# Optimization experiments

Hardware: AMD Instinct MI355X
Metric: run time of the kernel (lower is better)

## Reference

```python
import jax, jax.numpy as jnp
import numpy as np

H = 8          # num_heads
SPARSITY = 0.1


def setup_inputs() -> dict:
    key = jax.random.key(0)
    ks = jax.random.split(key, 16)
    B, S, D = 2, 2048, 1024
    g2 = H * H  # 64, distill width
    std = 0.02
    inp = {
        "x":   jax.random.normal(ks[0], (B, S, D), dtype=jnp.float32),
        "Wq":  jax.random.normal(ks[1], (D, D)) * std, "bq": jnp.zeros((D,)),
        "Wk":  jax.random.normal(ks[2], (D, D)) * std, "bk": jnp.zeros((D,)),
        "Wv":  jax.random.normal(ks[3], (D, D)) * std, "bv": jnp.zeros((D,)),
        "Wo":  jax.random.normal(ks[4], (D, D)) * std, "bo": jnp.zeros((D,)),
        "Wd":  jax.random.normal(ks[5], (g2, g2)) * std, "bd": jnp.zeros((g2,)),
        "Wg":  jax.random.normal(ks[6], (g2, D)) * std,  "bg": jnp.zeros((g2,)),
        "Wgp": jax.random.normal(ks[7], (D, g2)) * std,  "bgp": jnp.zeros((D,)),
    }
    return inp


def reference(x, Wq, bq, Wk, bk, Wv, bv, Wo, bo, Wd, bd, Wg, bg, Wgp, bgp):
    B, S, D = x.shape
    Dh = D // H
    scale = Dh ** -0.5
    k = max(int(S * SPARSITY), 1)

    def heads(W, b):  # [B,S,D] -> [B,H,S,Dh]
        return (x @ W.T + b).reshape(B, S, H, Dh).transpose(0, 2, 1, 3)

    Q, K, V = heads(Wq, bq), heads(Wk, bk), heads(Wv, bv)

    scores = jnp.einsum("bhqd,bhkd->bhqk", Q, K) * scale       # [B,H,S,S]
    # per-row top-k threshold (k-th largest value of each query row)
    thr = jax.lax.top_k(scores, k)[0][..., k - 1:k]              # [B,H,S,1]
    masked = jnp.where(scores >= thr, scores, -jnp.inf)
    probs = jax.nn.softmax(masked, axis=-1)
    attn = jnp.einsum("bhqk,bhkd->bhqd", probs, V)               # [B,H,S,Dh]
    attn = attn.transpose(0, 2, 1, 3).reshape(B, S, D)           # [B,S,D]

    g2 = H * H
    distilled = (attn.reshape(-1, g2) @ Wd.T + bd).reshape(B, S, D)

    gate = jax.nn.sigmoid(x.mean(axis=1) @ Wg.T + bg)            # [B,g2]
    gate = (gate @ Wgp.T + bgp)[:, None, :]                      # [B,1,D]

    mixed = gate * distilled + (1.0 - gate) * attn
    return mixed @ Wo.T + bo
```

## Files before the change

kernel.cpp:

```cpp
#include <hip/hip_runtime.h>

typedef __attribute__((ext_vector_type(8))) short bf16x8;
typedef __attribute__((ext_vector_type(4))) float f32x4;
typedef __attribute__((ext_vector_type(4))) unsigned int u32x4;

#define DEVINL __device__ __forceinline__

DEVINL unsigned short f2bf(float f){
  unsigned int u = __float_as_uint(f);
  unsigned int r = (u + 0x7FFFu + ((u >> 16) & 1u)) >> 16;
  return (unsigned short)r;
}
DEVINL float bf2f(unsigned short h){ return __uint_as_float(((unsigned int)h) << 16); }
DEVINL unsigned int fkey(float f){
  unsigned int u = __float_as_uint(f);
  return (u & 0x80000000u) ? ~u : (u | 0x80000000u);
}
DEVINL float fkeyinv(unsigned int k){
  unsigned int u = (k & 0x80000000u) ? (k & 0x7FFFFFFFu) : ~k;
  return __uint_as_float(u);
}
DEVINL unsigned int cvtpk(float lo, float hi){
  unsigned int r;
  asm("v_cvt_pk_bf16_f32 %0, %1, %2" : "=v"(r) : "v"(lo), "v"(hi));
  return r;
}

__global__ void prep_split_kernel(const float* __restrict__ src,
                                  unsigned short* __restrict__ hi,
                                  unsigned short* __restrict__ lo, int n){
  int i = blockIdx.x * 256 + threadIdx.x;
  if (i >= n) return;
  float f = src[i];
  unsigned short h = f2bf(f);
  hi[i] = h;
  if (lo) lo[i] = f2bf(f - bf2f(h));
}

template<bool SPLIT, int EPI>
__global__ __launch_bounds__(256) void gemm_kernel(
    const unsigned short* __restrict__ Ah, const unsigned short* __restrict__ Al,
    const unsigned short* __restrict__ Bh, const unsigned short* __restrict__ Bl,
    const float* __restrict__ bias0, const float* __restrict__ bias1, const float* __restrict__ bias2,
    unsigned short* __restrict__ qh, unsigned short* __restrict__ ql,
    unsigned short* __restrict__ kh, unsigned short* __restrict__ kl,
    unsigned short* __restrict__ vT, float* __restrict__ outf)
{
  const int K = 1024;
  __shared__ __align__(16) unsigned short sAh[128*40];
  __shared__ __align__(16) unsigned short sBh[128*40];
  __shared__ __align__(16) unsigned short sAl[SPLIT ? 128*40 : 8];
  __shared__ __align__(16) unsigned short sBl[SPLIT ? 128*40 : 8];

  const int tid = threadIdx.x;
  const int lane = tid & 63;
  const int w = tid >> 6;
  const int wr = w >> 1, wc = w & 1;
  const int l16 = lane & 15, lg = lane >> 4;
  const int bm = blockIdx.x, bn = blockIdx.y;

  f32x4 acc[4][4];
  #pragma unroll
  for (int i = 0; i < 4; i++)
    #pragma unroll
    for (int j = 0; j < 4; j++)
      acc[i][j] = (f32x4){0.f,0.f,0.f,0.f};

  for (int kt = 0; kt < K/32; ++kt){
    __syncthreads();
    #pragma unroll
    for (int c = 0; c < 2; c++){
      int lin = tid*16 + c*8;
      int row = lin >> 5, col = lin & 31;
      *(bf16x8*)&sAh[row*40+col] = *(const bf16x8*)&Ah[(size_t)(bm*128+row)*K + kt*32 + col];
      *(bf16x8*)&sBh[row*40+col] = *(const bf16x8*)&Bh[(size_t)(bn*128+row)*K + kt*32 + col];
      if constexpr (SPLIT){
        *(bf16x8*)&sAl[row*40+col] = *(const bf16x8*)&Al[(size_t)(bm*128+row)*K + kt*32 + col];
        *(bf16x8*)&sBl[row*40+col] = *(const bf16x8*)&Bl[(size_t)(bn*128+row)*K + kt*32 + col];
      }
    }
    __syncthreads();

    bf16x8 afh[4], afl[4], bfh[4], bfl[4];
    #pragma unroll
    for (int mi = 0; mi < 4; mi++){
      int off = (wr*64 + mi*16 + l16)*40 + lg*8;
      afh[mi] = *(const bf16x8*)&sAh[off];
      if constexpr (SPLIT) afl[mi] = *(const bf16x8*)&sAl[off];
    }
    #pragma unroll
    for (int ni = 0; ni < 4; ni++){
      int off = (wc*64 + ni*16 + l16)*40 + lg*8;
      bfh[ni] = *(const bf16x8*)&sBh[off];
      if constexpr (SPLIT) bfl[ni] = *(const bf16x8*)&sBl[off];
    }
    #pragma unroll
    for (int mi = 0; mi < 4; mi++)
      #pragma unroll
      for (int ni = 0; ni < 4; ni++){
        acc[mi][ni] = __builtin_amdgcn_mfma_f32_16x16x32_bf16(afh[mi], bfh[ni], acc[mi][ni], 0, 0, 0);
        if constexpr (SPLIT){
          acc[mi][ni] = __builtin_amdgcn_mfma_f32_16x16x32_bf16(afh[mi], bfl[ni], acc[mi][ni], 0, 0, 0);
          acc[mi][ni] = __builtin_amdgcn_mfma_f32_16x16x32_bf16(afl[mi], bfh[ni], acc[mi][ni], 0, 0, 0);
        }
      }
  }

  if constexpr (EPI == 0){
    const int wsel = (bn * 128) >> 10;
    const float* bias = (wsel == 0) ? bias0 : (wsel == 1) ? bias1 : bias2;
    #pragma unroll
    for (int mi = 0; mi < 4; mi++)
      #pragma unroll
      for (int ni = 0; ni < 4; ni++)
        #pragma unroll
        for (int i = 0; i < 4; i++){
          int m = bm*128 + wr*64 + mi*16 + lg*4 + i;
          int ng = bn*128 + wc*64 + ni*16 + l16;
          int n = ng & 1023;
          float v = acc[mi][ni][i] + bias[n];
          int b = m >> 11, s = m & 2047;
          int h = n >> 7, dh = n & 127;
          size_t base = (size_t)(b*8 + h)*262144;
          if (wsel == 2){
            size_t off = base + (size_t)(s>>5)*4096 + (dh>>4)*512
                       + (size_t)((((s>>3)&3)*16 + (dh&15))*8 + (s&7));
            vT[off] = f2bf(v);
          } else {
            size_t off = base + (size_t)(s>>4)*2048 + (dh>>5)*512
                       + (size_t)((((dh>>3)&3)*16 + (s&15))*8 + (dh&7));
            unsigned short hv = f2bf(v);
            if (wsel == 0){ qh[off] = hv; ql[off] = f2bf(v - bf2f(hv)); }
            else          { kh[off] = hv; kl[off] = f2bf(v - bf2f(hv)); }
          }
        }
  } else {
    #pragma unroll
    for (int mi = 0; mi < 4; mi++)
      #pragma unroll
      for (int ni = 0; ni < 4; ni++)
        #pragma unroll
        for (int i = 0; i < 4; i++){
          int m = bm*128 + wr*64 + mi*16 + lg*4 + i;
          int n = bn*128 + wc*64 + ni*16 + l16;
          outf[(size_t)m*1024 + n] = acc[mi][ni][i] + bias0[n];
        }
  }
}

__global__ __launch_bounds__(512, 4) void attn_kernel(
    const unsigned short* __restrict__ qh, const unsigned short* __restrict__ ql,
    const unsigned short* __restrict__ kh, const unsigned short* __restrict__ kl,
    const unsigned short* __restrict__ vT, float* __restrict__ attn_out)
{
  __shared__ __align__(16) float red[8][16][132];
  __shared__ float rpartm[8][16], rpartd[8][16];
  __shared__ unsigned int prefixv[16], kremv[16];
  unsigned int* hist = (unsigned int*)red;

  const int tid = threadIdx.x;
  const int lane = tid & 63;
  const int w = tid >> 6;
  const int l16 = lane & 15, lg = lane >> 4;
  const int swz = (blockIdx.x & 7) * 256 + (blockIdx.x >> 3);
  const int bh = swz >> 7, qb = swz & 127;
  const float scale = 0.08838834764831845f;

  const size_t base = (size_t)bh*262144;

  const size_t qpb = base + (size_t)qb*2048 + lane*8;
  bf16x8 aqh[4], aql[4];
  #pragma unroll
  for (int kk = 0; kk < 4; kk++){
    aqh[kk] = *(const bf16x8*)&qh[qpb + kk*512];
    aql[kk] = *(const bf16x8*)&ql[qpb + kk*512];
  }

  f32x4 acc[16];
  #pragma unroll
  for (int nt = 0; nt < 16; nt++){
    f32x4 a0 = (f32x4){0.f,0.f,0.f,0.f};
    f32x4 a1 = (f32x4){0.f,0.f,0.f,0.f};
    const size_t kb = base + (size_t)(w*16 + nt)*2048 + lane*8;
    __builtin_amdgcn_s_setprio(1);
    #pragma unroll
    for (int kk = 0; kk < 4; kk++){
      bf16x8 kbh = *(const bf16x8*)&kh[kb + kk*512];
      bf16x8 kbl = *(const bf16x8*)&kl[kb + kk*512];
      a0 = __builtin_amdgcn_mfma_f32_16x16x32_bf16(kbh, aqh[kk], a0, 0, 0, 0);
      a1 = __builtin_amdgcn_mfma_f32_16x16x32_bf16(kbh, aql[kk], a1, 0, 0, 0);
      a1 = __builtin_amdgcn_mfma_f32_16x16x32_bf16(kbl, aqh[kk], a1, 0, 0, 0);
    }
    __builtin_amdgcn_s_setprio(0);
    #pragma unroll
    for (int i = 0; i < 4; i++) acc[nt][i] = (a0[i] + a1[i]) * scale;
  }

  {
    float rm = -3.4e38f;
    #pragma unroll
    for (int nt = 0; nt < 16; nt++)
      #pragma unroll
      for (int i = 0; i < 4; i++) rm = fmaxf(rm, acc[nt][i]);
    rm = fmaxf(rm, __shfl_xor(rm, 16, 64));
    rm = fmaxf(rm, __shfl_xor(rm, 32, 64));
    if (lane < 16) rpartm[w][lane] = rm;
  }
  if (tid < 16){ prefixv[tid] = 0u; kremv[tid] = 204u; }

  #pragma unroll
  for (int nt = 0; nt < 16; nt++)
    #pragma unroll
    for (int i = 0; i < 4; i++)
      acc[nt][i] = __uint_as_float(fkey(acc[nt][i]));

  const int hco = (w >> 1) * (16*257);
  for (int pass = 3; pass >= 0; pass--){
    const int shift = pass*8;
    __syncthreads();
    for (int j = tid; j < 4*16*257; j += 512) hist[j] = 0u;
    __syncthreads();
    const unsigned int pf = prefixv[l16];
    const unsigned int mhi = (pass == 3) ? 0u : (0xFFFFFFFFu << (shift + 8));
    #pragma unroll
    for (int nt = 0; nt < 16; nt++)
      #pragma unroll
      for (int i = 0; i < 4; i++){
        unsigned int u = __float_as_uint(acc[nt][i]);
        if ((u & mhi) == pf)
          atomicAdd(&hist[hco + l16*257 + ((u >> shift) & 255u)], 1u);
      }
    __syncthreads();
    #pragma unroll
    for (int rr = 0; rr < 2; rr++){
      int r = w*2 + rr;
      unsigned int krem = kremv[r];
      unsigned int pfx  = prefixv[r];
      unsigned int cl[4], s4 = 0;
      #pragma unroll
      for (int t = 0; t < 4; t++){
        int idx = r*257 + 255 - 4*lane - t;
        cl[t] = hist[idx] + hist[16*257 + idx] + hist[2*16*257 + idx] + hist[3*16*257 + idx];
        s4 += cl[t];
      }
      unsigned int inc = s4;
      #pragma unroll
      for (int off = 1; off < 64; off <<= 1){
        unsigned int v = __shfl_up((int)inc, off, 64);
        if (lane >= off) inc += v;
      }
      unsigned int cb = inc - s4;
      #pragma unroll
      for (int t = 0; t < 4; t++){
        if (krem > cb && krem <= cb + cl[t]){
          int d = 255 - 4*lane - t;
          prefixv[r] = pfx | ((unsigned int)d << shift);
          kremv[r]   = krem - cb;
        }
        cb += cl[t];
      }
    }
  }
  __syncthreads();

  const unsigned int th = prefixv[l16];
  float rmax = rpartm[0][l16];
  #pragma unroll
  for (int w8 = 1; w8 < 8; w8++) rmax = fmaxf(rmax, rpartm[w8][l16]);
  const int src01 = ((lg & 1) << 5) + l16;
  const int src23 = src01 + 16;
  const size_t vb0 = base + (size_t)(w*8)*4096 + lane*8;
  float dn = 0.f;
  f32x4 pacc[8];
  #pragma unroll
  for (int dt = 0; dt < 8; dt++) pacc[dt] = (f32x4){0.f,0.f,0.f,0.f};
  #pragma unroll
  for (int t = 0; t < 8; t++){
    float p[8];
    #pragma unroll
    for (int j = 0; j < 4; j++){
      unsigned int u = __float_as_uint(acc[2*t][j]);
      p[j] = (u >= th) ? __expf(fkeyinv(u) - rmax) : 0.f;
    }
    #pragma unroll
    for (int j = 0; j < 4; j++){
      unsigned int u = __float_as_uint(acc[2*t+1][j]);
      p[4+j] = (u >= th) ? __expf(fkeyinv(u) - rmax) : 0.f;
    }
    unsigned int d0 = cvtpk(p[0], p[1]), d1 = cvtpk(p[2], p[3]);
    unsigned int d2 = cvtpk(p[4], p[5]), d3 = cvtpk(p[6], p[7]);
    dn += __uint_as_float(d0 << 16) + __uint_as_float(d0 & 0xFFFF0000u)
        + __uint_as_float(d1 << 16) + __uint_as_float(d1 & 0xFFFF0000u)
        + __uint_as_float(d2 << 16) + __uint_as_float(d2 & 0xFFFF0000u)
        + __uint_as_float(d3 << 16) + __uint_as_float(d3 & 0xFFFF0000u);
    unsigned int A0 = (unsigned int)__shfl((int)d0, src01, 64);
    unsigned int A1 = (unsigned int)__shfl((int)d1, src01, 64);
    unsigned int A2 = (unsigned int)__shfl((int)d0, src23, 64);
    unsigned int A3 = (unsigned int)__shfl((int)d1, src23, 64);
    unsigned int B0 = (unsigned int)__shfl((int)d2, src01, 64);
    unsigned int B1 = (unsigned int)__shfl((int)d3, src01, 64);
    unsigned int B2 = (unsigned int)__shfl((int)d2, src23, 64);
    unsigned int B3 = (unsigned int)__shfl((int)d3, src23, 64);
    u32x4 pdv = (lg < 2) ? (u32x4){A0, A1, A2, A3} : (u32x4){B0, B1, B2, B3};
    bf16x8 pa = __builtin_bit_cast(bf16x8, pdv);
    __builtin_amdgcn_s_setprio(1);
    #pragma unroll
    for (int dt = 0; dt < 8; dt++){
      bf16x8 bv = *(const bf16x8*)&vT[vb0 + (size_t)t*4096 + dt*512];
      pacc[dt] = __builtin_amdgcn_mfma_f32_16x16x32_bf16(pa, bv, pacc[dt], 0, 0, 0);
    }
    __builtin_amdgcn_s_setprio(0);
  }
  dn += __shfl_xor(dn, 16, 64);
  dn += __shfl_xor(dn, 32, 64);
  if (lane < 16) rpartd[w][lane] = dn;

  #pragma unroll
  for (int dt = 0; dt < 8; dt++)
    #pragma unroll
    for (int i = 0; i < 4; i++)
      red[w][lg*4 + i][dt*16 + l16] = pacc[dt][i];
  __syncthreads();

  {
    const int q = tid >> 5;
    const int c0 = (tid & 31) * 4;
    f32x4 s0 = (f32x4){0.f,0.f,0.f,0.f};
    #pragma unroll
    for (int w8 = 0; w8 < 8; w8++)
      s0 += *(const f32x4*)&red[w8][q][c0];
    float dnm = 0.f;
    #pragma unroll
    for (int w8 = 0; w8 < 8; w8++) dnm += rpartd[w8][q];
    const int b = bh >> 3, h = bh & 7;
    float* op = &attn_out[((size_t)b*2048 + qb*16 + q)*1024 + h*128 + c0];
    f32x4 o0;
    #pragma unroll
    for (int i = 0; i < 4; i++) o0[i] = s0[i] / dnm;
    *(f32x4*)op = o0;
  }
}

__global__ void mean_partial_kernel(const float* __restrict__ x, float* __restrict__ partial){
  int b = blockIdx.x >> 5, scn = blockIdx.x & 31;
  int tid = threadIdx.x;
  #pragma unroll
  for (int dc = 0; dc < 4; dc++){
    int d = dc*256 + tid;
    float s = 0.f;
    for (int ss = 0; ss < 64; ss++) s += x[((size_t)b*2048 + scn*64 + ss)*1024 + d];
    partial[((size_t)b*32 + scn)*1024 + d] = s;
  }
}

__global__ __launch_bounds__(256) void gate_kernel(const float* __restrict__ partial,
    const float* __restrict__ Wg, const float* __restrict__ bg,
    const float* __restrict__ Wgp, const float* __restrict__ bgp,
    float* __restrict__ gate){
  __shared__ float xm[2][1024];
  __shared__ float gb[2][64];
  int tid = threadIdx.x;
  for (int idx = tid; idx < 2048; idx += 256){
    int b = idx >> 10, d = idx & 1023;
    float s = 0.f;
    for (int scn = 0; scn < 32; scn++) s += partial[((size_t)b*32 + scn)*1024 + d];
    xm[b][d] = s * (1.f/2048.f);
  }
  __syncthreads();
  if (tid < 128){
    int b = tid >> 6, j = tid & 63;
    float s = bg[j];
    for (int d = 0; d < 1024; d++) s += xm[b][d] * Wg[j*1024 + d];
    gb[b][j] = 1.f / (1.f + __expf(-s));
  }
  __syncthreads();
  for (int idx = tid; idx < 2048; idx += 256){
    int b = idx >> 10, d = idx & 1023;
    float s = bgp[d];
    for (int j = 0; j < 64; j++) s += gb[b][j] * Wgp[d*64 + j];
    gate[idx] = s;
  }
}

__global__ __launch_bounds__(256) void mix_kernel(const float* __restrict__ attn,
    const float* __restrict__ Wd, const float* __restrict__ bd,
    const float* __restrict__ gate,
    unsigned short* __restrict__ mixedh, unsigned short* __restrict__ mixedl){
  __shared__ float sWdT[64*64];
  __shared__ float arow[1024];
  int tid = threadIdx.x;
  for (int i = tid; i < 4096; i += 256){
    int m = i >> 6, cc = i & 63;
    sWdT[i] = Wd[cc*64 + m];
  }
  int rbase = blockIdx.x * 16;
  for (int rr = 0; rr < 16; rr++){
    int row = rbase + rr;
    __syncthreads();
    for (int i = tid; i < 1024; i += 256) arow[i] = attn[(size_t)row*1024 + i];
    __syncthreads();
    int b = row >> 11;
    #pragma unroll
    for (int c4 = 0; c4 < 4; c4++){
      int dcol = c4*256 + tid;
      int j = dcol >> 6, cc = dcol & 63;
      float y = bd[cc];
      for (int m = 0; m < 64; m++) y += arow[j*64 + m] * sWdT[m*64 + cc];
      float g = gate[b*1024 + dcol];
      float mv = g*y + (1.f - g)*arow[dcol];
      unsigned short hv = f2bf(mv);
      mixedh[(size_t)row*1024 + dcol] = hv;
      mixedl[(size_t)row*1024 + dcol] = f2bf(mv - bf2f(hv));
    }
  }
}

extern "C" void kernel_launch(void* const* d_in, const int* in_sizes, int n_in,
                              void* d_out, int out_size, void* d_ws, size_t ws_size,
                              hipStream_t stream){
  (void)in_sizes; (void)n_in; (void)out_size; (void)ws_size;
  const float* x   = (const float*)d_in[0];
  const float* Wq  = (const float*)d_in[1];
  const float* bq  = (const float*)d_in[2];
  const float* Wk  = (const float*)d_in[3];
  const float* bk  = (const float*)d_in[4];
  const float* Wv  = (const float*)d_in[5];
  const float* bv  = (const float*)d_in[6];
  const float* Wo  = (const float*)d_in[7];
  const float* bo  = (const float*)d_in[8];
  const float* Wd  = (const float*)d_in[9];
  const float* bd  = (const float*)d_in[10];
  const float* Wg  = (const float*)d_in[11];
  const float* bg  = (const float*)d_in[12];
  const float* Wgp = (const float*)d_in[13];
  const float* bgp = (const float*)d_in[14];
  float* out = (float*)d_out;

  const size_t MiB = 1048576;
  char* ws = (char*)d_ws;
  unsigned short* xh     = (unsigned short*)(ws + 0*MiB);
  unsigned short* xl     = (unsigned short*)(ws + 8*MiB);
  float*          attnws = (float*)(ws + 0*MiB);
  unsigned short* whi    = (unsigned short*)(ws + 16*MiB);
  unsigned short* wlo    = (unsigned short*)(ws + 22*MiB);
  unsigned short* wohi   = (unsigned short*)(ws + 16*MiB);
  unsigned short* wolo   = (unsigned short*)(ws + 18*MiB);
  float*          partial= (float*)(ws + 20*MiB);
  float*          gatews = (float*)(ws + 20*MiB + 262144);
  unsigned short* qh_    = (unsigned short*)(ws + 28*MiB);
  unsigned short* ql_    = (unsigned short*)(ws + 36*MiB);
  unsigned short* mixedh = (unsigned short*)(ws + 28*MiB);
  unsigned short* mixedl = (unsigned short*)(ws + 36*MiB);
  unsigned short* kh_    = (unsigned short*)(ws + 44*MiB);
  unsigned short* kl_    = (unsigned short*)(ws + 52*MiB);
  unsigned short* vT_    = (unsigned short*)(ws + 60*MiB);

  prep_split_kernel<<<16384, 256, 0, stream>>>(x,  xh, xl, 4194304);
  prep_split_kernel<<<4096,  256, 0, stream>>>(Wq, whi,           wlo,           1048576);
  prep_split_kernel<<<4096,  256, 0, stream>>>(Wk, whi + 1048576, wlo + 1048576, 1048576);
  prep_split_kernel<<<4096,  256, 0, stream>>>(Wv, whi + 2097152, wlo + 2097152, 1048576);

  gemm_kernel<true, 0><<<dim3(32, 24), 256, 0, stream>>>(
      xh, xl, whi, wlo, bq, bk, bv, qh_, ql_, kh_, kl_, vT_, nullptr);

  prep_split_kernel<<<4096,  256, 0, stream>>>(Wo, wohi, wolo, 1048576);

  attn_kernel<<<2048, 512, 0, stream>>>(qh_, ql_, kh_, kl_, vT_, attnws);

  mean_partial_kernel<<<64, 256, 0, stream>>>(x, partial);
  gate_kernel<<<1, 256, 0, stream>>>(partial, Wg, bg, Wgp, bgp, gatews);

  mix_kernel<<<256, 256, 0, stream>>>(attnws, Wd, bd, gatews, mixedh, mixedl);

  gemm_kernel<true, 1><<<dim3(32, 8), 256, 0, stream>>>(
      mixedh, mixedl, wohi, wolo, bo, nullptr, nullptr,
      nullptr, nullptr, nullptr, nullptr, nullptr, out);
}
```

Measured before the change: 494.3 us.

## Use direct global-to-LDS loads in GEMM and parallelize gate computation

The GEMM tile loads now go through global_load_lds, which writes from global memory straight into LDS without passing through registers. The padded 40-element LDS row stride becomes an unpadded 32, which may add bank conflicts on the fragment reads. The gate path is also split: the mean reduction uses 256 blocks instead of 64, and the single-block gate kernel becomes two kernels that use wave-level shuffle reductions and vectorized weight loads, removing a serial one-block bottleneck.

After: 473.8 us. 4.1% less time.

```diff
diff --git a/kernel.cpp b/kernel.cpp
--- a/kernel.cpp
+++ b/kernel.cpp
@@ -24,6 +24,10 @@
   unsigned int r;
   asm("v_cvt_pk_bf16_f32 %0, %1, %2" : "=v"(r) : "v"(lo), "v"(hi));
   return r;
+}
+DEVINL void gload16(void* lds, const void* g){
+  __builtin_amdgcn_global_load_lds((const __attribute__((address_space(1))) void*)g,
+                                   (__attribute__((address_space(3))) void*)lds, 16, 0, 0);
 }
 
 __global__ void prep_split_kernel(const float* __restrict__ src,
@@ -47,10 +51,10 @@
     unsigned short* __restrict__ vT, float* __restrict__ outf)
 {
   const int K = 1024;
-  __shared__ __align__(16) unsigned short sAh[128*40];
-  __shared__ __align__(16) unsigned short sBh[128*40];
-  __shared__ __align__(16) unsigned short sAl[SPLIT ? 128*40 : 8];
-  __shared__ __align__(16) unsigned short sBl[SPLIT ? 128*40 : 8];
+  __shared__ __align__(16) unsigned short sAh[128*32];
+  __shared__ __align__(16) unsigned short sBh[128*32];
+  __shared__ __align__(16) unsigned short sAl[SPLIT ? 128*32 : 8];
+  __shared__ __align__(16) unsigned short sBl[SPLIT ? 128*32 : 8];
 
   const int tid = threadIdx.x;
   const int lane = tid & 63;
@@ -59,6 +63,10 @@
   const int l16 = lane & 15, lg = lane >> 4;
   const int bm = blockIdx.x, bn = blockIdx.y;
 
+  const int srow = (lane >> 2);
+  const int scol = (lane & 3) * 8;
+  const int r0 = w * 32;
+
   f32x4 acc[4][4];
   #pragma unroll
   for (int i = 0; i < 4; i++)
@@ -69,14 +77,14 @@
   for (int kt = 0; kt < K/32; ++kt){
     __syncthreads();
     #pragma unroll
-    for (int c = 0; c < 2; c++){
-      int lin = tid*16 + c*8;
-      int row = lin >> 5, col = lin & 31;
-      *(bf16x8*)&sAh[row*40+col] = *(const bf16x8*)&Ah[(size_t)(bm*128+row)*K + kt*32 + col];
-      *(bf16x8*)&sBh[row*40+col] = *(const bf16x8*)&Bh[(size_t)(bn*128+row)*K + kt*32 + col];
+    for (int cc = 0; cc < 2; cc++){
+      const int rr = r0 + cc*16 + srow;
+      const int lb = (r0 + cc*16) * 32;
+      gload16(&sAh[lb], &Ah[(size_t)(bm*128 + rr)*K + kt*32 + scol]);
+      gload16(&sBh[lb], &Bh[(size_t)(bn*128 + rr)*K + kt*32 + scol]);
       if constexpr (SPLIT){
-        *(bf16x8*)&sAl[row*40+col] = *(const bf16x8*)&Al[(size_t)(bm*128+row)*K + kt*32 + col];
-        *(bf16x8*)&sBl[row*40+col] = *(const bf16x8*)&Bl[(size_t)(bn*128+row)*K + kt*32 + col];
+        gload16(&sAl[lb], &Al[(size_t)(bm*128 + rr)*K + kt*32 + scol]);
+        gload16(&sBl[lb], &Bl[(size_t)(bn*128 + rr)*K + kt*32 + scol]);
       }
     }
     __syncthreads();
@@ -84,13 +92,13 @@
     bf16x8 afh[4], afl[4], bfh[4], bfl[4];
     #pragma unroll
     for (int mi = 0; mi < 4; mi++){
-      int off = (wr*64 + mi*16 + l16)*40 + lg*8;
+      int off = (wr*64 + mi*16 + l16)*32 + lg*8;
       afh[mi] = *(const bf16x8*)&sAh[off];
       if constexpr (SPLIT) afl[mi] = *(const bf16x8*)&sAl[off];
     }
     #pragma unroll
     for (int ni = 0; ni < 4; ni++){
-      int off = (wc*64 + ni*16 + l16)*40 + lg*8;
+      int off = (wc*64 + ni*16 + l16)*32 + lg*8;
       bfh[ni] = *(const bf16x8*)&sBh[off];
       if constexpr (SPLIT) bfl[ni] = *(const bf16x8*)&sBl[off];
     }
@@ -342,44 +350,58 @@
 }
 
 __global__ void mean_partial_kernel(const float* __restrict__ x, float* __restrict__ partial){
-  int b = blockIdx.x >> 5, scn = blockIdx.x & 31;
+  int b = blockIdx.x >> 7, ch = blockIdx.x & 127;
   int tid = threadIdx.x;
   #pragma unroll
   for (int dc = 0; dc < 4; dc++){
     int d = dc*256 + tid;
     float s = 0.f;
-    for (int ss = 0; ss < 64; ss++) s += x[((size_t)b*2048 + scn*64 + ss)*1024 + d];
-    partial[((size_t)b*32 + scn)*1024 + d] = s;
-  }
-}
-
-__global__ __launch_bounds__(256) void gate_kernel(const float* __restrict__ partial,
-    const float* __restrict__ Wg, const float* __restrict__ bg,
-    const float* __restrict__ Wgp, const float* __restrict__ bgp,
-    float* __restrict__ gate){
-  __shared__ float xm[2][1024];
-  __shared__ float gb[2][64];
-  int tid = threadIdx.x;
-  for (int idx = tid; idx < 2048; idx += 256){
-    int b = idx >> 10, d = idx & 1023;
+    for (int ss = 0; ss < 16; ss++) s += x[((size_t)b*2048 + ch*16 + ss)*1024 + d];
+    partial[((size_t)b*128 + ch)*1024 + d] = s;
+  }
+}
+
+__global__ __launch_bounds__(512) void gate_sig_kernel(const float* __restrict__ partial,
+    const float* __restrict__ Wg, const float* __restrict__ bg, float* __restrict__ gsig){
+  __shared__ float xm[1024];
+  const int b = blockIdx.x;
+  const int tid = threadIdx.x, lane = tid & 63, w = tid >> 6;
+  for (int d = tid; d < 1024; d += 512){
     float s = 0.f;
-    for (int scn = 0; scn < 32; scn++) s += partial[((size_t)b*32 + scn)*1024 + d];
-    xm[b][d] = s * (1.f/2048.f);
+    for (int c = 0; c < 128; c++) s += partial[((size_t)b*128 + c)*1024 + d];
+    xm[d] = s * (1.f/2048.f);
   }
   __syncthreads();
-  if (tid < 128){
-    int b = tid >> 6, j = tid & 63;
-    float s = bg[j];
-    for (int d = 0; d < 1024; d++) s += xm[b][d] * Wg[j*1024 + d];
-    gb[b][j] = 1.f / (1.f + __expf(-s));
-  }
+  for (int jj = 0; jj < 8; jj++){
+    const int j = w*8 + jj;
+    float s = 0.f;
+    #pragma unroll
+    for (int c = 0; c < 4; c++){
+      f32x4 wv = *(const f32x4*)&Wg[(size_t)j*1024 + lane*16 + c*4];
+      s += wv[0]*xm[lane*16 + c*4] + wv[1]*xm[lane*16 + c*4 + 1]
+         + wv[2]*xm[lane*16 + c*4 + 2] + wv[3]*xm[lane*16 + c*4 + 3];
+    }
+    #pragma unroll
+    for (int off = 1; off < 64; off <<= 1) s += __shfl_xor(s, off, 64);
+    if (lane == 0) gsig[b*64 + j] = 1.f / (1.f + __expf(-(s + bg[j])));
+  }
+}
+
+__global__ __launch_bounds__(256) void gate_proj_kernel(const float* __restrict__ gsig,
+    const float* __restrict__ Wgp, const float* __restrict__ bgp, float* __restrict__ gate){
+  __shared__ float gb[64];
+  const int blk = blockIdx.x;
+  const int b = blk >> 2;
+  const int d = (blk & 3) * 256 + threadIdx.x;
+  if (threadIdx.x < 64) gb[threadIdx.x] = gsig[b*64 + threadIdx.x];
   __syncthreads();
-  for (int idx = tid; idx < 2048; idx += 256){
-    int b = idx >> 10, d = idx & 1023;
-    float s = bgp[d];
-    for (int j = 0; j < 64; j++) s += gb[b][j] * Wgp[d*64 + j];
-    gate[idx] = s;
-  }
+  float s = bgp[d];
+  #pragma unroll
+  for (int j4 = 0; j4 < 16; j4++){
+    f32x4 wv = *(const f32x4*)&Wgp[(size_t)d*64 + j4*4];
+    s += wv[0]*gb[j4*4] + wv[1]*gb[j4*4+1] + wv[2]*gb[j4*4+2] + wv[3]*gb[j4*4+3];
+  }
+  gate[b*1024 + d] = s;
 }
 
 __global__ __launch_bounds__(256) void mix_kernel(const float* __restrict__ attn,
@@ -446,7 +468,8 @@
   unsigned short* wohi   = (unsigned short*)(ws + 16*MiB);
   unsigned short* wolo   = (unsigned short*)(ws + 18*MiB);
   float*          partial= (float*)(ws + 20*MiB);
-  float*          gatews = (float*)(ws + 20*MiB + 262144);
+  float*          gatews = (float*)(ws + 21*MiB);
+  float*          gsig   = (float*)(ws + 21*MiB + 16384);
   unsigned short* qh_    = (unsigned short*)(ws + 28*MiB);
   unsigned short* ql_    = (unsigned short*)(ws + 36*MiB);
   unsigned short* mixedh = (unsigned short*)(ws + 28*MiB);
@@ -467,8 +490,9 @@
 
   attn_kernel<<<2048, 512, 0, stream>>>(qh_, ql_, kh_, kl_, vT_, attnws);
 
-  mean_partial_kernel<<<64, 256, 0, stream>>>(x, partial);
-  gate_kernel<<<1, 256, 0, stream>>>(partial, Wg, bg, Wgp, bgp, gatews);
+  mean_partial_kernel<<<256, 256, 0, stream>>>(x, partial);
+  gate_sig_kernel<<<2, 512, 0, stream>>>(partial, Wg, bg, gsig);
+  gate_proj_kernel<<<8, 256, 0, stream>>>(gsig, Wgp, bgp, gatews);
 
   mix_kernel<<<256, 256, 0, stream>>>(attnws, Wd, bd, gatews, mixedh, mixedl);
 
```
